# Optimization experiments

Hardware: AMD Instinct MI355X
Metric: run time of the kernel (lower is better)

Reference implementation:

```python
import jax, jax.numpy as jnp
import numpy as np

NEG_SLOPE = 0.2
EPS = 1e-6


def setup_inputs() -> dict:
    key = jax.random.key(0)
    k1, k2 = jax.random.split(key)
    B, C, N = 4, 64, 32768
    x = jax.random.normal(k1, (B, C, 3, N), dtype=jnp.float32)
    # VNLinear weight: nn.Linear(in, out, bias=False).weight -> [out, in]
    W = jax.random.normal(k2, (C, C), dtype=jnp.float32) * (1.0 / np.sqrt(C))
    return {"x": x, "W": W}


def reference(x, W):
    # VNLinear: kron(W, eye(3)) conv2d == per-3-vector channel mix
    # d[b,o,v,n] = sum_i W[o,i] * x[b,i,v,n]
    d = jnp.einsum('oi,bivn->bovn', W, x)
    dotprod = jnp.sum(x * d, axis=2, keepdims=True)      # [B,C,1,N]
    d_norm_sq = jnp.sum(d * d, axis=2, keepdims=True)    # [B,C,1,N]
    neg = x - (1.0 - NEG_SLOPE) * (dotprod / (d_norm_sq + EPS)) * d
    return jnp.where(dotprod >= 0, x, neg)
```

## Files before the change

### kernel.cpp

```cpp
#include <hip/hip_runtime.h>

#define NEG_SLOPE 0.2f
#define EPS 1e-6f


#define C_CH 64
#define V_DIM 3
#define N_FULL 32768
#define NT 64
#define THREADS 512

typedef __attribute__((ext_vector_type(8))) short bf16x8;
typedef __attribute__((ext_vector_type(4))) float f32x4;

__device__ __forceinline__ ushort f2bf(float f) {
    union { float f; unsigned u; } v; v.f = f;
    unsigned r = v.u + 0x7FFFu + ((v.u >> 16) & 1u);
    return (ushort)(r >> 16);
}
__device__ __forceinline__ float bf2f(ushort s) {
    union { unsigned u; float f; } v; v.u = ((unsigned)s) << 16; return v.f;
}
__device__ __forceinline__ unsigned f2u(float f) {
    union { float f; unsigned u; } v; v.f = f; return v.u;
}
__device__ __forceinline__ float u2f(unsigned u) {
    union { unsigned u; float f; } v; v.u = u; return v.f;
}

__global__ void w_split_kernel(const float* __restrict__ W,
                               ushort* __restrict__ whi, ushort* __restrict__ wlo) {
    int i = blockIdx.x * 256 + threadIdx.x;
    if (i < C_CH * C_CH) {
        float w = W[i];
        ushort h = f2bf(w);
        whi[i] = h;
        wlo[i] = f2bf(w - bf2f(h));
    }
}

template<bool USE_WS>
__global__ __launch_bounds__(THREADS, 6)
void vn_dma64(const float* __restrict__ x,
              const float* __restrict__ Wf,
              const ushort* __restrict__ whi, const ushort* __restrict__ wlo,
              float* __restrict__ out) {
    __shared__ float xs[V_DIM * C_CH][NT];

    const int t    = threadIdx.x;
    const int tile = blockIdx.x;
    const int b    = tile >> 9;
    const int n0   = (tile & 511) << 6;

    const float* xb = x + (size_t)b * (C_CH * V_DIM * N_FULL) + n0;

    const int lane = t & 63;
    const int w    = t >> 6;
    const int wo   = w >> 2;
    const int wn   = w & 3;
    const int l4   = lane & 15;
    const int hi   = lane >> 4;

    #pragma unroll
    for (int it = 0; it < 6; ++it) {
        int r = 4 * (w * 6 + it) + (lane >> 4);
        int i = (r * 171) >> 9;
        int chunk = (lane & 15) ^ (((i >> 3) & 3) << 2);
        const float* g = xb + (size_t)r * N_FULL + (chunk << 2);
        void* l = (char*)(&xs[0][0]) + (size_t)(w * 6 + it) * 1024 + (size_t)lane * 16;
        __builtin_amdgcn_global_load_lds(
            (const __attribute__((address_space(1))) unsigned*)g,
            (__attribute__((address_space(3))) unsigned*)l, 16, 0, 0);
    }

    bf16x8 Ah[2][2], Al[2][2];
    if (USE_WS) {
        #pragma unroll
        for (int m = 0; m < 2; ++m)
            #pragma unroll
            for (int kh = 0; kh < 2; ++kh) {
                size_t off = (size_t)(wo * 32 + m * 16 + l4) * C_CH + kh * 32 + hi * 8;
                Ah[m][kh] = *(const bf16x8*)(whi + off);
                Al[m][kh] = *(const bf16x8*)(wlo + off);
            }
    } else {
        #pragma unroll
        for (int m = 0; m < 2; ++m)
            #pragma unroll
            for (int kh = 0; kh < 2; ++kh) {
                const float* wp = Wf + (size_t)(wo * 32 + m * 16 + l4) * C_CH + kh * 32 + hi * 8;
                float4 wa = *(const float4*)wp;
                float4 wb = *(const float4*)(wp + 4);
                float wf[8] = {wa.x, wa.y, wa.z, wa.w, wb.x, wb.y, wb.z, wb.w};
                bf16x8 h, l;
                #pragma unroll
                for (int j = 0; j < 8; ++j) {
                    ushort hb = f2bf(wf[j]);
                    h[j] = (short)hb;
                    l[j] = (short)f2bf(wf[j] - bf2f(hb));
                }
                Ah[m][kh] = h; Al[m][kh] = l;
            }
    }

    __syncthreads();

    f32x4 acc[2][3];
    #pragma unroll
    for (int m = 0; m < 2; ++m)
        #pragma unroll
        for (int v = 0; v < 3; ++v)
            acc[m][v] = (f32x4){0.f, 0.f, 0.f, 0.f};

    const int acol = (wn * 16 + l4) ^ (hi << 4);
    #pragma unroll
    for (int v = 0; v < 3; ++v) {
        #pragma unroll
        for (int kh = 0; kh < 2; ++kh) {
            const int ib = kh * 32 + hi * 8;
            float f[8];
            #pragma unroll
            for (int j = 0; j < 8; ++j)
                f[j] = xs[3 * (ib + j) + v][acol];
            union { bf16x8 v8; unsigned d[4]; } BH, BL;
            unsigned rl[8];
            #pragma unroll
            for (int j = 0; j < 8; ++j)
                rl[j] = f2u(f[j] - u2f(f2u(f[j]) & 0xffff0000u));
            #pragma unroll
            for (int q = 0; q < 4; ++q) {
                BH.d[q] = __builtin_amdgcn_perm(f2u(f[2 * q + 1]), f2u(f[2 * q]), 0x07060302u);
                BL.d[q] = __builtin_amdgcn_perm(rl[2 * q + 1], rl[2 * q], 0x07060302u);
            }
            #pragma unroll
            for (int m = 0; m < 2; ++m) {
                acc[m][v] = __builtin_amdgcn_mfma_f32_16x16x32_bf16(Ah[m][kh], BH.v8, acc[m][v], 0, 0, 0);
                acc[m][v] = __builtin_amdgcn_mfma_f32_16x16x32_bf16(Ah[m][kh], BL.v8, acc[m][v], 0, 0, 0);
                acc[m][v] = __builtin_amdgcn_mfma_f32_16x16x32_bf16(Al[m][kh], BH.v8, acc[m][v], 0, 0, 0);
            }
        }
    }

    const int n = wn * 16 + l4;
    float* ob = out + (size_t)b * (C_CH * V_DIM * N_FULL) + n0 + n;
    #pragma unroll
    for (int m = 0; m < 2; ++m) {
        #pragma unroll
        for (int rr = 0; rr < 4; ++rr) {
            const int o = wo * 32 + m * 16 + hi * 4 + rr;
            const int ecol = n ^ (((m * 2 + (hi >> 1)) & 3) << 4);
            float xv[3], dv[3];
            #pragma unroll
            for (int v = 0; v < 3; ++v) {
                xv[v] = xs[3 * o + v][ecol];
                dv[v] = acc[m][v][rr];
            }
            float dot  = xv[0] * dv[0] + xv[1] * dv[1] + xv[2] * dv[2];
            float dnsq = dv[0] * dv[0] + dv[1] * dv[1] + dv[2] * dv[2];
            float f = (1.0f - NEG_SLOPE) * dot * __builtin_amdgcn_rcpf(dnsq + EPS);
            f = (dot >= 0.f) ? 0.f : f;
            float o0 = fmaf(-f, dv[0], xv[0]);
            float o1 = fmaf(-f, dv[1], xv[1]);
            float o2 = fmaf(-f, dv[2], xv[2]);
            float* op = ob + (size_t)o * (V_DIM * N_FULL);
            op[0 * N_FULL] = o0;
            op[1 * N_FULL] = o1;
            op[2 * N_FULL] = o2;
        }
    }
}

extern "C" void kernel_launch(void* const* d_in, const int* in_sizes, int n_in,
                              void* d_out, int out_size, void* d_ws, size_t ws_size,
                              hipStream_t stream) {
    const float* x = (const float*)d_in[0];
    const float* W = (const float*)d_in[1];
    float* out = (float*)d_out;

    const int B = 4;
    const int blocks = B * (N_FULL / NT);

    if (ws_size >= 2u * C_CH * C_CH * sizeof(ushort)) {
        ushort* whi = (ushort*)d_ws;
        ushort* wlo = whi + C_CH * C_CH;
        w_split_kernel<<<(C_CH * C_CH + 255) / 256, 256, 0, stream>>>(W, whi, wlo);
        vn_dma64<true><<<blocks, THREADS, 0, stream>>>(x, W, whi, wlo, out);
    } else {
        vn_dma64<false><<<blocks, THREADS, 0, stream>>>(x, W, nullptr, nullptr, out);
    }
}
```

Measured before the change: 46.32 us.

## Drop LDS staging and load x tiles directly from global memory

Removes the shared-memory tile and the async global-to-LDS copy plus barrier. Each lane now reads its MFMA operands and epilogue x values straight from global memory, relying on cache for reuse. The tile shrinks to 32 columns with 256-thread blocks, doubling the block count. Each lane's reads are 64-byte column segments rather than wide vector loads, and every x element is read twice (once for the MFMA operand, once in the epilogue), adding global/cache traffic on a memory-bound kernel.

```diff
diff --git a/kernel.cpp b/kernel.cpp
--- a/kernel.cpp
+++ b/kernel.cpp
@@ -7,8 +7,7 @@
 #define C_CH 64
 #define V_DIM 3
 #define N_FULL 32768
-#define NT 64
-#define THREADS 512
+#define THREADS 256
 
 typedef __attribute__((ext_vector_type(8))) short bf16x8;
 typedef __attribute__((ext_vector_type(4))) float f32x4;
@@ -41,37 +40,24 @@
 
 template<bool USE_WS>
 __global__ __launch_bounds__(THREADS, 6)
-void vn_dma64(const float* __restrict__ x,
+void vn_nolds(const float* __restrict__ x,
               const float* __restrict__ Wf,
               const ushort* __restrict__ whi, const ushort* __restrict__ wlo,
               float* __restrict__ out) {
-    __shared__ float xs[V_DIM * C_CH][NT];
-
     const int t    = threadIdx.x;
     const int tile = blockIdx.x;
-    const int b    = tile >> 9;
-    const int n0   = (tile & 511) << 6;
+    const int b    = tile >> 10;
+    const int n0   = (tile & 1023) << 5;
 
     const float* xb = x + (size_t)b * (C_CH * V_DIM * N_FULL) + n0;
 
     const int lane = t & 63;
     const int w    = t >> 6;
-    const int wo   = w >> 2;
-    const int wn   = w & 3;
+    const int wo   = w >> 1;
+    const int wn   = w & 1;
     const int l4   = lane & 15;
     const int hi   = lane >> 4;
-
-    #pragma unroll
-    for (int it = 0; it < 6; ++it) {
-        int r = 4 * (w * 6 + it) + (lane >> 4);
-        int i = (r * 171) >> 9;
-        int chunk = (lane & 15) ^ (((i >> 3) & 3) << 2);
-        const float* g = xb + (size_t)r * N_FULL + (chunk << 2);
-        void* l = (char*)(&xs[0][0]) + (size_t)(w * 6 + it) * 1024 + (size_t)lane * 16;
-        __builtin_amdgcn_global_load_lds(
-            (const __attribute__((address_space(1))) unsigned*)g,
-            (__attribute__((address_space(3))) unsigned*)l, 16, 0, 0);
-    }
+    const int n    = wn * 16 + l4;
 
     bf16x8 Ah[2][2], Al[2][2];
     if (USE_WS) {
@@ -103,8 +89,6 @@
             }
     }
 
-    __syncthreads();
-
     f32x4 acc[2][3];
     #pragma unroll
     for (int m = 0; m < 2; ++m)
@@ -112,16 +96,15 @@
         for (int v = 0; v < 3; ++v)
             acc[m][v] = (f32x4){0.f, 0.f, 0.f, 0.f};
 
-    const int acol = (wn * 16 + l4) ^ (hi << 4);
+    const float* bb = xb + (size_t)(hi * 8) * (V_DIM * N_FULL) + n;
     #pragma unroll
     for (int v = 0; v < 3; ++v) {
         #pragma unroll
         for (int kh = 0; kh < 2; ++kh) {
-            const int ib = kh * 32 + hi * 8;
             float f[8];
             #pragma unroll
             for (int j = 0; j < 8; ++j)
-                f[j] = xs[3 * (ib + j) + v][acol];
+                f[j] = bb[(size_t)(kh * 96 + 3 * j + v) * N_FULL];
             union { bf16x8 v8; unsigned d[4]; } BH, BL;
             unsigned rl[8];
             #pragma unroll
@@ -141,18 +124,17 @@
         }
     }
 
-    const int n = wn * 16 + l4;
     float* ob = out + (size_t)b * (C_CH * V_DIM * N_FULL) + n0 + n;
     #pragma unroll
     for (int m = 0; m < 2; ++m) {
         #pragma unroll
         for (int rr = 0; rr < 4; ++rr) {
             const int o = wo * 32 + m * 16 + hi * 4 + rr;
-            const int ecol = n ^ (((m * 2 + (hi >> 1)) & 3) << 4);
+            const float* ep = xb + (size_t)(o * 3) * N_FULL + n;
             float xv[3], dv[3];
             #pragma unroll
             for (int v = 0; v < 3; ++v) {
-                xv[v] = xs[3 * o + v][ecol];
+                xv[v] = ep[(size_t)v * N_FULL];
                 dv[v] = acc[m][v][rr];
             }
             float dot  = xv[0] * dv[0] + xv[1] * dv[1] + xv[2] * dv[2];
@@ -178,14 +160,14 @@
     float* out = (float*)d_out;
 
     const int B = 4;
-    const int blocks = B * (N_FULL / NT);
+    const int blocks = B * (N_FULL / 32);
 
     if (ws_size >= 2u * C_CH * C_CH * sizeof(ushort)) {
         ushort* whi = (ushort*)d_ws;
         ushort* wlo = whi + C_CH * C_CH;
         w_split_kernel<<<(C_CH * C_CH + 255) / 256, 256, 0, stream>>>(W, whi, wlo);
-        vn_dma64<true><<<blocks, THREADS, 0, stream>>>(x, W, whi, wlo, out);
+        vn_nolds<true><<<blocks, THREADS, 0, stream>>>(x, W, whi, wlo, out);
     } else {
-        vn_dma64<false><<<blocks, THREADS, 0, stream>>>(x, W, nullptr, nullptr, out);
+        vn_nolds<false><<<blocks, THREADS, 0, stream>>>(x, W, nullptr, nullptr, out);
     }
 }
```

Result: slower. 62.48 us (+34.9%).
